# Optimization experiments

Measured on AMD Instinct MI355X. Metric: run time of the kernel, lower is better.

Reference implementation:

```python
import jax, jax.numpy as jnp
import numpy as np


def setup_inputs() -> dict:
    key = jax.random.key(0)
    k1, k2 = jax.random.split(key)
    N, H, W, F = 32, 16, 16, 256
    B, C = 64, 8
    x = jax.random.normal(k1, (N, H, W, F), dtype=jnp.float32)
    # keras 'uniform' initializer: U(-0.05, 0.05)
    T = jax.random.uniform(k2, (F, B, C), dtype=jnp.float32, minval=-0.05, maxval=0.05)
    return {"x": x, "T": T}


def reference(x, T):
    # x: [N,H,W,F], T: [F,B,C]
    M = jnp.einsum('nhwf,fbc->nhwbc', x, T)            # [N,H,W,B,C]
    # all-pairs L1 distance over C between samples i and j
    diff = jnp.abs(M[:, None] - M[None, :])            # [N,N,H,W,B,C]
    norm = jnp.sum(diff, axis=-1)                      # [N,N,H,W,B]
    o_b = jnp.sum(jnp.exp(-norm), axis=1)              # [N,H,W,B]
    return jnp.concatenate([x, o_b], axis=3)           # [N,H,W,F+B]
```

## Files before the change

kernel.cpp:

```cpp
#include <hip/hip_runtime.h>
#include <hip/hip_bf16.h>


namespace {
constexpr int kN = 32;
constexpr int kHW = 256;
constexpr int kF = 256;
constexpr int kOutRow = 320;
constexpr int kMstride = 136;
constexpr int kOstride = 24;
}

using frag_ab = __attribute__((ext_vector_type(8))) short;
using frag_cd = __attribute__((ext_vector_type(4))) float;
typedef _Float16 h2 __attribute__((ext_vector_type(2)));

__device__ inline unsigned short f2bf(float f) {
  union { __hip_bfloat16 h; unsigned short u; } c;
  c.h = __float2bfloat16(f);
  return c.u;
}

__device__ inline h2 absd2(unsigned a, unsigned b) {
  h2 d = __builtin_bit_cast(h2, a) - __builtin_bit_cast(h2, b);
  return __builtin_bit_cast(h2, __builtin_bit_cast(unsigned, d) & 0x7fff7fffu);
}

__device__ inline float l1_8(const uint4& a, const uint4& b) {
  h2 s01 = absd2(a.x, b.x) + absd2(a.y, b.y);
  h2 s23 = absd2(a.z, b.z) + absd2(a.w, b.w);
  h2 s = s01 + s23;
  return (float)s.x + (float)s.y;
}

__global__ __launch_bounds__(256)
void pack_T(const float* __restrict__ T, uint4* __restrict__ Tf) {
  const int g = blockIdx.x * 256 + threadIdx.x;
  const int l = g & 63;
  const int frag = g >> 6;
  const int tt = frag >> 3, kt = frag & 7;
  const int col = tt * 16 + (l & 15);
  const int k0 = kt * 32 + (l >> 4) * 8;
  unsigned p[4];
#pragma unroll
  for (int jj = 0; jj < 4; ++jj) {
    float a = T[(size_t)(k0 + jj * 2) * 512 + col];
    float b = T[(size_t)(k0 + jj * 2 + 1) * 512 + col];
    p[jj] = (unsigned)f2bf(a) | ((unsigned)f2bf(b) << 16);
  }
  Tf[g] = make_uint4(p[0], p[1], p[2], p[3]);
}

__global__ __launch_bounds__(256, 4)
void mbd_main(const float* __restrict__ x, const uint4* __restrict__ Tf,
              float* __restrict__ out) {
  __shared__ uint4 Afrag[2 * 8 * 64];
  __shared__ __align__(16) unsigned short Mlds[kN * kMstride];
  float* obuf = (float*)Afrag;
  const int hw = blockIdx.x & (kHW - 1);
  const int qg = blockIdx.x >> 8;
  const int tid = threadIdx.x;
  const int l = tid & 63, w = tid >> 6;

  uint4 bfr[2][8];
#pragma unroll
  for (int q = 0; q < 2; ++q)
#pragma unroll
    for (int kt = 0; kt < 8; ++kt) {
      const int tT = qg * 8 + w * 2 + q;
      bfr[q][kt] = Tf[(tT * 8 + kt) * 64 + l];
    }

  const float4* x4 = (const float4*)x;
  float4* out4 = (float4*)out;
#pragma unroll
  for (int s = 0; s < 4; ++s) {
    const int task = tid + s * 256;
    const int n = task >> 5;
    const int k8 = task & 31;
    const size_t xb = (size_t)n * (kHW * kF / 4) + (size_t)hw * (kF / 4) + k8 * 2;
    float4 v0 = x4[xb];
    float4 v1 = x4[xb + 1];
    if ((k8 >> 3) == qg) {
      const size_t ob = (size_t)(n * kHW + hw) * (kOutRow / 4) + k8 * 2;
      out4[ob] = v0;
      out4[ob + 1] = v1;
    }
    uint4 p;
    p.x = (unsigned)f2bf(v0.x) | ((unsigned)f2bf(v0.y) << 16);
    p.y = (unsigned)f2bf(v0.z) | ((unsigned)f2bf(v0.w) << 16);
    p.z = (unsigned)f2bf(v1.x) | ((unsigned)f2bf(v1.y) << 16);
    p.w = (unsigned)f2bf(v1.z) | ((unsigned)f2bf(v1.w) << 16);
    const int rt = n >> 4, kt = k8 >> 2, ln = (n & 15) | ((k8 & 3) << 4);
    Afrag[(rt * 8 + kt) * 64 + ln] = p;
  }
  __syncthreads();

  frag_cd acc[2][2] = {};
#pragma unroll
  for (int kt = 0; kt < 8; ++kt) {
    uint4 a0 = Afrag[(0 * 8 + kt) * 64 + l];
    uint4 a1 = Afrag[(1 * 8 + kt) * 64 + l];
    frag_ab af0 = __builtin_bit_cast(frag_ab, a0);
    frag_ab af1 = __builtin_bit_cast(frag_ab, a1);
#pragma unroll
    for (int q = 0; q < 2; ++q) {
      frag_ab bf = __builtin_bit_cast(frag_ab, bfr[q][kt]);
      acc[q][0] = __builtin_amdgcn_mfma_f32_16x16x32_bf16(af0, bf, acc[q][0], 0, 0, 0);
      acc[q][1] = __builtin_amdgcn_mfma_f32_16x16x32_bf16(af1, bf, acc[q][1], 0, 0, 0);
    }
  }

#pragma unroll
  for (int q = 0; q < 2; ++q)
#pragma unroll
    for (int rt = 0; rt < 2; ++rt)
#pragma unroll
      for (int r = 0; r < 4; ++r) {
        const int n = rt * 16 + (l >> 4) * 4 + r;
        const int t = (w * 2 + q) * 16 + (l & 15);
        Mlds[n * kMstride + t] =
            __builtin_bit_cast(unsigned short, (_Float16)acc[q][rt][r]);
      }
  __syncthreads();

  const int b = tid >> 4;
  const int i0 = (tid & 15) * 2;
  const uint4 mi0 = *(const uint4*)&Mlds[i0 * kMstride + b * 8];
  const uint4 mi1 = *(const uint4*)&Mlds[(i0 + 1) * kMstride + b * 8];
  float ob0 = 0.f, ob1 = 0.f;
#pragma unroll 8
  for (int j = 0; j < kN; ++j) {
    const uint4 mj = *(const uint4*)&Mlds[j * kMstride + b * 8];
    ob0 += __expf(-l1_8(mi0, mj));
    ob1 += __expf(-l1_8(mi1, mj));
  }
  obuf[i0 * kOstride + b] = ob0;
  obuf[(i0 + 1) * kOstride + b] = ob1;
  __syncthreads();

  if (tid < 128) {
    const int n = tid >> 2;
    const int b4 = tid & 3;
    float4 v = *(const float4*)&obuf[n * kOstride + b4 * 4];
    out4[(size_t)(n * kHW + hw) * (kOutRow / 4) + (kF / 4) + qg * 4 + b4] = v;
  }
}

extern "C" void kernel_launch(void* const* d_in, const int* in_sizes, int n_in,
                              void* d_out, int out_size, void* d_ws, size_t ws_size,
                              hipStream_t stream) {
  const float* x = (const float*)d_in[0];
  const float* T = (const float*)d_in[1];
  float* out = (float*)d_out;
  uint4* Tf = (uint4*)d_ws;
  (void)in_sizes; (void)n_in; (void)out_size; (void)ws_size;
  pack_T<<<dim3(64), dim3(256), 0, stream>>>(T, Tf);
  mbd_main<<<dim3(4 * kHW), dim3(256), 0, stream>>>(x, Tf, out);
}
```

Measured before the change: 76.66 us.

## Double block size to 512 threads, one B tile per wave, stream T fragments

Each block now runs 512 threads (8 waves), so each wave owns a single 16-column T tile instead of two. The per-wave register preload of 16 T fragments is replaced by a one-ahead streamed load inside the MFMA loop. The pairwise L1 stage now assigns one sample per thread instead of two. The aim is to cut register pressure and raise parallelism and latency hiding per block, at the cost of more threads sharing LDS and less work per thread.

```diff
diff --git a/kernel.cpp b/kernel.cpp
--- a/kernel.cpp
+++ b/kernel.cpp
@@ -51,7 +51,7 @@
   Tf[g] = make_uint4(p[0], p[1], p[2], p[3]);
 }
 
-__global__ __launch_bounds__(256, 4)
+__global__ __launch_bounds__(512, 8)
 void mbd_main(const float* __restrict__ x, const uint4* __restrict__ Tf,
               float* __restrict__ out) {
   __shared__ uint4 Afrag[2 * 8 * 64];
@@ -62,20 +62,14 @@
   const int tid = threadIdx.x;
   const int l = tid & 63, w = tid >> 6;
 
-  uint4 bfr[2][8];
-#pragma unroll
-  for (int q = 0; q < 2; ++q)
-#pragma unroll
-    for (int kt = 0; kt < 8; ++kt) {
-      const int tT = qg * 8 + w * 2 + q;
-      bfr[q][kt] = Tf[(tT * 8 + kt) * 64 + l];
-    }
+  const uint4* tf0 = Tf + (size_t)(qg * 8 + w) * 512 + l;
+  uint4 bq = tf0[0];
 
   const float4* x4 = (const float4*)x;
   float4* out4 = (float4*)out;
 #pragma unroll
-  for (int s = 0; s < 4; ++s) {
-    const int task = tid + s * 256;
+  for (int s = 0; s < 2; ++s) {
+    const int task = tid + s * 512;
     const int n = task >> 5;
     const int k8 = task & 31;
     const size_t xb = (size_t)n * (kHW * kF / 4) + (size_t)hw * (kF / 4) + k8 * 2;
@@ -96,47 +90,42 @@
   }
   __syncthreads();
 
-  frag_cd acc[2][2] = {};
+  frag_cd acc[2] = {};
+  uint4 nb;
 #pragma unroll
   for (int kt = 0; kt < 8; ++kt) {
+    if (kt < 7) nb = tf0[(kt + 1) * 64];
     uint4 a0 = Afrag[(0 * 8 + kt) * 64 + l];
     uint4 a1 = Afrag[(1 * 8 + kt) * 64 + l];
     frag_ab af0 = __builtin_bit_cast(frag_ab, a0);
     frag_ab af1 = __builtin_bit_cast(frag_ab, a1);
-#pragma unroll
-    for (int q = 0; q < 2; ++q) {
-      frag_ab bf = __builtin_bit_cast(frag_ab, bfr[q][kt]);
-      acc[q][0] = __builtin_amdgcn_mfma_f32_16x16x32_bf16(af0, bf, acc[q][0], 0, 0, 0);
-      acc[q][1] = __builtin_amdgcn_mfma_f32_16x16x32_bf16(af1, bf, acc[q][1], 0, 0, 0);
-    }
+    frag_ab bf = __builtin_bit_cast(frag_ab, bq);
+    acc[0] = __builtin_amdgcn_mfma_f32_16x16x32_bf16(af0, bf, acc[0], 0, 0, 0);
+    acc[1] = __builtin_amdgcn_mfma_f32_16x16x32_bf16(af1, bf, acc[1], 0, 0, 0);
+    bq = nb;
   }
 
 #pragma unroll
-  for (int q = 0; q < 2; ++q)
+  for (int rt = 0; rt < 2; ++rt)
 #pragma unroll
-    for (int rt = 0; rt < 2; ++rt)
-#pragma unroll
-      for (int r = 0; r < 4; ++r) {
-        const int n = rt * 16 + (l >> 4) * 4 + r;
-        const int t = (w * 2 + q) * 16 + (l & 15);
-        Mlds[n * kMstride + t] =
-            __builtin_bit_cast(unsigned short, (_Float16)acc[q][rt][r]);
-      }
+    for (int r = 0; r < 4; ++r) {
+      const int n = rt * 16 + (l >> 4) * 4 + r;
+      const int t = w * 16 + (l & 15);
+      Mlds[n * kMstride + t] =
+          __builtin_bit_cast(unsigned short, (_Float16)acc[rt][r]);
+    }
   __syncthreads();
 
-  const int b = tid >> 4;
-  const int i0 = (tid & 15) * 2;
-  const uint4 mi0 = *(const uint4*)&Mlds[i0 * kMstride + b * 8];
-  const uint4 mi1 = *(const uint4*)&Mlds[(i0 + 1) * kMstride + b * 8];
-  float ob0 = 0.f, ob1 = 0.f;
+  const int b = tid >> 5;
+  const int i = tid & 31;
+  const uint4 mi = *(const uint4*)&Mlds[i * kMstride + b * 8];
+  float ob = 0.f;
 #pragma unroll 8
   for (int j = 0; j < kN; ++j) {
     const uint4 mj = *(const uint4*)&Mlds[j * kMstride + b * 8];
-    ob0 += __expf(-l1_8(mi0, mj));
-    ob1 += __expf(-l1_8(mi1, mj));
+    ob += __expf(-l1_8(mi, mj));
   }
-  obuf[i0 * kOstride + b] = ob0;
-  obuf[(i0 + 1) * kOstride + b] = ob1;
+  obuf[i * kOstride + b] = ob;
   __syncthreads();
 
   if (tid < 128) {
@@ -156,5 +145,5 @@
   uint4* Tf = (uint4*)d_ws;
   (void)in_sizes; (void)n_in; (void)out_size; (void)ws_size;
   pack_T<<<dim3(64), dim3(256), 0, stream>>>(T, Tf);
-  mbd_main<<<dim3(4 * kHW), dim3(256), 0, stream>>>(x, Tf, out);
+  mbd_main<<<dim3(4 * kHW), dim3(512), 0, stream>>>(x, Tf, out);
 }
```

Result: no change. 75.96 us (-0.9%).
